# Optimization experiments

Hardware: AMD Instinct MI355X
Metric: run time of the kernel (lower is better)

The kernel has to match this reference:

```python
import jax, jax.numpy as jnp
import numpy as np

K = 16          # knn_graph k
FPS_RATIO = 0.5 # fps ratio
BN_EPS = 1e-5


def knn_idx(p, k):
    # p: [B, N, 3] -> neighbor indices [B, N, k] (loop=True: self included)
    n2 = jnp.sum(p * p, axis=-1)                                  # [B, N]
    d = n2[:, :, None] + n2[:, None, :] - 2.0 * jnp.einsum('bnc,bmc->bnm', p, p)
    _, idx = jax.lax.top_k(-d, k)                                 # smallest distances
    return idx


def gather_nbrs(x, idx):
    # x: [B, N, C], idx: [B, N, k] -> [B, N, k, C]
    return jax.vmap(lambda xb, ib: xb[ib])(x, idx)


def bn_silu(y, g, be):
    # training-mode BatchNorm over all rows (flattened) + SiLU, per PyG MLP defaults
    C = y.shape[-1]
    yf = y.reshape(-1, C)
    mu = jnp.mean(yf, axis=0)
    var = jnp.mean((yf - mu) ** 2, axis=0)
    return jax.nn.silu((y - mu) * jax.lax.rsqrt(var + BN_EPS) * g + be)


def fps_idx(p, m):
    # farthest point sampling on one cloud p: [N, 3], deterministic start at 0
    d0 = jnp.sum((p - p[0]) ** 2, axis=-1)
    def step(mind, _):
        i = jnp.argmax(mind)
        di = jnp.sum((p - p[i]) ** 2, axis=-1)
        return jnp.minimum(mind, di), i.astype(jnp.int32)
    _, idxs = jax.lax.scan(step, d0, None, length=m - 1)
    return jnp.concatenate([jnp.zeros((1,), jnp.int32), idxs])


def setup_inputs() -> dict:
    key = jax.random.key(0)
    ks = jax.random.split(key, 4)
    B, N, zdim = 16, 2048, 256
    return {
        'pos': jax.random.normal(ks[0], (B, N, 3), jnp.float32),
        'W1': jax.random.normal(ks[1], (6, 64), jnp.float32) * (1.0 / np.sqrt(6)),
        'b1': jnp.zeros((64,), jnp.float32),
        'g1': jnp.ones((64,), jnp.float32),
        'be1': jnp.zeros((64,), jnp.float32),
        'W2a': jax.random.normal(ks[2], (67, 128), jnp.float32) * (1.0 / np.sqrt(67)),
        'b2a': jnp.zeros((128,), jnp.float32),
        'g2a': jnp.ones((128,), jnp.float32),
        'be2a': jnp.zeros((128,), jnp.float32),
        'W2b': jax.random.normal(ks[3], (128, zdim), jnp.float32) * (1.0 / np.sqrt(128)),
        'b2b': jnp.zeros((zdim,), jnp.float32),
        'g2b': jnp.ones((zdim,), jnp.float32),
        'be2b': jnp.zeros((zdim,), jnp.float32),
    }


def reference(pos, W1, b1, g1, be1, W2a, b2a, g2a, be2a, W2b, b2b, g2b, be2b):
    B, N, _ = pos.shape
    M = int(N * FPS_RATIO)

    # conv1: knn graph on pos, message = MLP([x_j, pos_j - pos_i]), max-aggr
    idx1 = knn_idx(pos, K)                                  # [B, N, K]
    pos_j = gather_nbrs(pos, idx1)                          # [B, N, K, 3]
    msg = jnp.concatenate([pos_j, pos_j - pos[:, :, None, :]], axis=-1)  # [B,N,K,6]
    h = bn_silu(msg @ W1 + b1, g1, be1)                     # [B, N, K, 64]
    h = jnp.max(h, axis=2)                                  # [B, N, 64]

    # farthest point sampling, ratio 0.5
    idx_f = jax.vmap(fps_idx, in_axes=(0, None))(pos, M)    # [B, M]
    h = jax.vmap(lambda a, i: a[i])(h, idx_f)               # [B, M, 64]
    pos2 = jax.vmap(lambda a, i: a[i])(pos, idx_f)          # [B, M, 3]

    # conv2: knn on sampled points, message = MLP2([h_j, pos_j - pos_i]), max-aggr
    idx2 = knn_idx(pos2, K)                                 # [B, M, K]
    h_j = gather_nbrs(h, idx2)                              # [B, M, K, 64]
    p_j = gather_nbrs(pos2, idx2)                           # [B, M, K, 3]
    msg2 = jnp.concatenate([h_j, p_j - pos2[:, :, None, :]], axis=-1)  # [B,M,K,67]
    h2 = bn_silu(msg2 @ W2a + b2a, g2a, be2a)               # [B, M, K, 128]
    h2 = bn_silu(h2 @ W2b + b2b, g2b, be2b)                 # [B, M, K, zdim]
    h2 = jnp.max(h2, axis=2)                                # [B, M, zdim]

    # global max aggregation per cloud
    return jnp.max(h2, axis=1)                              # [B, zdim]
```

## Files before the change

kernel.cpp:

```cpp
#include <hip/hip_runtime.h>
#include <hip/hip_bf16.h>

#define NB 16
#define NN 2048
#define KNNK 16
#define MM 1024
#define RC1 (NB*NN*KNNK)
#define RC2 (NB*MM*KNNK)

typedef unsigned long long u64;
typedef __attribute__((ext_vector_type(8))) short short8;
typedef __attribute__((ext_vector_type(4))) float f32x4;

__device__ __forceinline__ float frn_mul(float a, float b){ return __fmul_rn(a,b); }
__device__ __forceinline__ float frn_add(float a, float b){ return __fadd_rn(a,b); }
__device__ __forceinline__ float frn_sub(float a, float b){ return __fsub_rn(a,b); }
__device__ __forceinline__ float silu_f(float x){ return x / (1.0f + __expf(-x)); }
__device__ __forceinline__ u64 umax64(u64 a, u64 b){ return a > b ? a : b; }

__device__ __forceinline__ unsigned f32_sortable(float f){
  unsigned u = __float_as_uint(f);
  return u ^ ((unsigned)((int)u >> 31) | 0x80000000u);
}
__device__ __forceinline__ unsigned short f2bf(float f){
  unsigned u = __float_as_uint(f);
  return (unsigned short)((u + 0x7FFFu + ((u >> 16) & 1u)) >> 16);
}
__device__ __forceinline__ float bf2f(unsigned short h){
  return __uint_as_float(((unsigned)h) << 16);
}

__device__ __forceinline__ void atomicMaxF(unsigned* addr, float v){
  if (v >= 0.f) atomicMax((int*)addr, (int)__float_as_uint(v));
  else          atomicMin(addr, __float_as_uint(v));
}
__device__ __forceinline__ void atomicMinF(unsigned* addr, float v){
  if (v >= 0.f) atomicMin((int*)addr, (int)__float_as_uint(v));
  else          atomicMax(addr, __float_as_uint(v));
}

__global__ __launch_bounds__(256) void init_kernel(float* stats1, float* stats2a, float* stats2b,
                                                   unsigned* gmax, unsigned* gmin){
  int t = blockIdx.x*256 + threadIdx.x;
  if (t < 128) stats1[t] = 0.f;
  if (t < 256) stats2a[t] = 0.f;
  if (t < 512) stats2b[t] = 0.f;
  if (t < 4096){ gmax[t] = 0xFF800000u; gmin[t] = 0x7F800000u; }
}

template<int CNT>
__device__ __forceinline__ void knn_scan(const float4* pts, int jbase,
                                         float xi, float yi, float zi, float n2i, u64* best){
#pragma unroll
  for (int p = 0; p < KNNK; ++p) best[p] = ~0ull;
  for (int jj = 0; jj < CNT; ++jj){
    float4 v = pts[jbase + jj];
    float e = frn_add(frn_add(frn_mul(xi,v.x), frn_mul(yi,v.y)), frn_mul(zi,v.z));
    float d = frn_sub(frn_add(n2i, v.w), frn_mul(2.0f, e));
    u64 key = ((u64)f32_sortable(d) << 32) | (unsigned)(jbase + jj);
    if (key < best[KNNK-1]){
      u64 cur = key;
#pragma unroll
      for (int p = 0; p < KNNK; ++p){
        u64 mn = best[p] < cur ? best[p] : cur;
        u64 mx = best[p] < cur ? cur : best[p];
        best[p] = mn; cur = mx;
      }
    }
  }
}

__global__ __launch_bounds__(256) void k0_fps_knn1(const float* __restrict__ pos,
    int* __restrict__ idxf, float* __restrict__ pos2, int* __restrict__ idx1,
    const float* __restrict__ W1, const float* __restrict__ b1, float* __restrict__ stats1){
  __shared__ __align__(16) char smem[74*1024];
  int tid = threadIdx.x;
  if (blockIdx.x < 16){
    int b = blockIdx.x;
    float4* pts4 = (float4*)smem;
    int* sel = (int*)(smem + 32*1024);
    u64* wred = (u64*)(smem + 36*1024);
    const float* pb = pos + (size_t)b*NN*3;
    float X[8], Y[8], Z[8], MD[8];
    unsigned LO[8];
#pragma unroll
    for (int q = 0; q < 8; ++q){
      int p = tid + 256*q;
      float x = pb[p*3+0], y = pb[p*3+1], z = pb[p*3+2];
      X[q] = x; Y[q] = y; Z[q] = z;
      LO[q] = ~(unsigned)p;
      pts4[p] = make_float4(x, y, z, 0.f);
    }
    float qx = pb[0], qy = pb[1], qz = pb[2];
#pragma unroll
    for (int q = 0; q < 8; ++q){
      float dx = frn_sub(X[q],qx), dy = frn_sub(Y[q],qy), dz = frn_sub(Z[q],qz);
      MD[q] = frn_add(frn_add(frn_mul(dx,dx), frn_mul(dy,dy)), frn_mul(dz,dz));
    }
    if (tid == 0) sel[0] = 0;
    int wv = tid >> 6;
    __syncthreads();
    for (int s = 1; s < MM; ++s){
      u64 t0 = umax64(((u64)__float_as_uint(MD[0])<<32)|LO[0], ((u64)__float_as_uint(MD[1])<<32)|LO[1]);
      u64 t1 = umax64(((u64)__float_as_uint(MD[2])<<32)|LO[2], ((u64)__float_as_uint(MD[3])<<32)|LO[3]);
      u64 t2 = umax64(((u64)__float_as_uint(MD[4])<<32)|LO[4], ((u64)__float_as_uint(MD[5])<<32)|LO[5]);
      u64 t3 = umax64(((u64)__float_as_uint(MD[6])<<32)|LO[6], ((u64)__float_as_uint(MD[7])<<32)|LO[7]);
      u64 kk = umax64(umax64(t0, t1), umax64(t2, t3));
#define RED_DPP(CTRL) { \
      unsigned lo_ = (unsigned)kk, hi_ = (unsigned)(kk>>32); \
      unsigned plo = (unsigned)__builtin_amdgcn_update_dpp((int)lo_,(int)lo_,CTRL,0xF,0xF,false); \
      unsigned phi = (unsigned)__builtin_amdgcn_update_dpp((int)hi_,(int)hi_,CTRL,0xF,0xF,false); \
      u64 o = ((u64)phi<<32)|plo; kk = o > kk ? o : kk; }
      RED_DPP(0xB1)
      RED_DPP(0x4E)
      RED_DPP(0x124)
      RED_DPP(0x128)
      RED_DPP(0x142)
      RED_DPP(0x143)
#undef RED_DPP
      int par = s & 1;
      if ((tid & 63) == 63) wred[par*4 + wv] = kk;
      __syncthreads();
      const u64* wr = wred + par*4;
      u64 K = umax64(umax64(wr[0], wr[1]), umax64(wr[2], wr[3]));
      unsigned wp = ~(unsigned)K;
      if (tid == 0) sel[s] = (int)wp;
      float4 wc = pts4[wp];
#pragma unroll
      for (int q = 0; q < 8; ++q){
        float dx = frn_sub(X[q],wc.x), dy = frn_sub(Y[q],wc.y), dz = frn_sub(Z[q],wc.z);
        float d = frn_add(frn_add(frn_mul(dx,dx), frn_mul(dy,dy)), frn_mul(dz,dz));
        MD[q] = fminf(MD[q], d);
      }
    }
    __syncthreads();
    for (int m = tid; m < MM; m += 256){
      int j = sel[m];
      idxf[b*MM + m] = j;
      float4 c = pts4[j];
      pos2[(size_t)(b*MM+m)*3+0] = c.x;
      pos2[(size_t)(b*MM+m)*3+1] = c.y;
      pos2[(size_t)(b*MM+m)*3+2] = c.z;
    }
  } else {
    int cid = blockIdx.x - 16;
    int b = cid >> 4;
    int rb16 = cid & 15;
    float4* pts4 = (float4*)smem;
    u64* cres = (u64*)(smem + 32*1024);
    int* idxl = (int*)(smem + 64*1024);
    float* red = (float*)(smem + 72*1024);
    const float* pb = pos + (size_t)b*NN*3;
    for (int i = tid; i < NN; i += 256){
      float x = pb[i*3+0], y = pb[i*3+1], z = pb[i*3+2];
      float n2 = frn_add(frn_add(frn_mul(x,x), frn_mul(y,y)), frn_mul(z,z));
      pts4[i] = make_float4(x, y, z, n2);
    }
    __syncthreads();
    int lrow = tid & 127;
    int ch = tid >> 7;
    int i = rb16*128 + lrow;
    float4 qv = pts4[i];
    u64 best[KNNK];
    knn_scan<1024>(pts4, ch*1024, qv.x, qv.y, qv.z, qv.w, best);
#pragma unroll
    for (int p = 0; p < KNNK; ++p) cres[tid*KNNK + p] = best[p];
    __syncthreads();
    if (tid < 128){
      const u64* A = cres + tid*KNNK;
      const u64* B = cres + (tid + 128)*KNNK;
      int ia = 0, ib = 0;
      int* op = idx1 + ((size_t)(b*NN + rb16*128 + tid))*KNNK;
#pragma unroll
      for (int p = 0; p < KNNK; ++p){
        u64 ka = A[ia], kb = B[ib];
        int v;
        if (ka < kb){ v = (int)(unsigned)ka; ++ia; }
        else        { v = (int)(unsigned)kb; ++ib; }
        op[p] = v;
        idxl[tid*KNNK + p] = v;
      }
    }
    __syncthreads();
    int lane = tid & 63, wv = tid >> 6;
    float w[6];
#pragma unroll
    for (int f = 0; f < 6; ++f) w[f] = W1[f*64 + lane];
    float bias = b1[lane];
    float ssum = 0.f, ssq = 0.f;
    for (int r = 0; r < 32; ++r){
      int lr = wv*32 + r;
      float4 pi = pts4[rb16*128 + lr];
      const int* ip = idxl + lr*KNNK;
#pragma unroll 4
      for (int k = 0; k < KNNK; ++k){
        int j = ip[k];
        float4 pj = pts4[j];
        float y = bias;
        y = fmaf(pj.x, w[0], y); y = fmaf(pj.y, w[1], y); y = fmaf(pj.z, w[2], y);
        y = fmaf(pj.x - pi.x, w[3], y); y = fmaf(pj.y - pi.y, w[4], y); y = fmaf(pj.z - pi.z, w[5], y);
        ssum += y; ssq = fmaf(y, y, ssq);
      }
    }
    red[(wv*64+lane)*2+0] = ssum; red[(wv*64+lane)*2+1] = ssq;
    __syncthreads();
    if (tid < 64){
      float s = red[(0*64+lane)*2]+red[(1*64+lane)*2]+red[(2*64+lane)*2]+red[(3*64+lane)*2];
      float q = red[(0*64+lane)*2+1]+red[(1*64+lane)*2+1]+red[(2*64+lane)*2+1]+red[(3*64+lane)*2+1];
      atomicAdd(&stats1[lane], s);
      atomicAdd(&stats1[64+lane], q);
    }
  }
}

__global__ __launch_bounds__(256) void k1_knn2_c1apply(
    const float* __restrict__ pos2, int* __restrict__ idx2,
    const float* __restrict__ pos, const int* __restrict__ idx1,
    const float* __restrict__ W1, const float* __restrict__ b1,
    const float* __restrict__ g1, const float* __restrict__ be1,
    const float* __restrict__ stats1, float* __restrict__ h){
  __shared__ __align__(16) char smem[48*1024];
  int tid = threadIdx.x;
  if (blockIdx.x < 256){
    int b = blockIdx.x >> 4;
    int rb = blockIdx.x & 15;
    float4* sm = (float4*)smem;
    u64* cres = (u64*)(smem + 16*1024);
    const float* pb = pos2 + (size_t)b*MM*3;
    for (int t = tid; t < MM; t += 256){
      float x = pb[t*3+0], y = pb[t*3+1], z = pb[t*3+2];
      float n2 = frn_add(frn_add(frn_mul(x,x), frn_mul(y,y)), frn_mul(z,z));
      sm[t] = make_float4(x, y, z, n2);
    }
    __syncthreads();
    int trow = tid & 63, ch = tid >> 6;
    int i = rb*64 + trow;
    float4 qv = sm[i];
    u64 best[KNNK];
    knn_scan<256>(sm, ch*256, qv.x, qv.y, qv.z, qv.w, best);
#pragma unroll
    for (int p = 0; p < KNNK; ++p) cres[tid*KNNK + p] = best[p];
    __syncthreads();
    if (tid < 64){
      const u64* L0 = cres + tid*KNNK;
      const u64* L1 = cres + (64 + tid)*KNNK;
      const u64* L2 = cres + (128 + tid)*KNNK;
      const u64* L3 = cres + (192 + tid)*KNNK;
      int o0=0, o1=0, o2=0, o3=0;
      int* op = idx2 + ((size_t)(b*MM + rb*64 + tid))*KNNK;
#pragma unroll
      for (int p = 0; p < KNNK; ++p){
        u64 k0 = L0[o0], k1 = L1[o1], k2 = L2[o2], k3 = L3[o3];
        u64 m01 = k0 < k1 ? k0 : k1;
        u64 m23 = k2 < k3 ? k2 : k3;
        u64 m = m01 < m23 ? m01 : m23;
        op[p] = (int)(unsigned)m;
        o0 += (m == k0); o1 += (m == k1); o2 += (m == k2); o3 += (m == k3);
      }
    }
  } else {
    int lane = tid & 63, wv = tid >> 6;
    int wave = (blockIdx.x - 256)*4 + wv;
    float w[6];
#pragma unroll
    for (int f = 0; f < 6; ++f) w[f] = W1[f*64 + lane];
    float bias = b1[lane];
    const float inv = 1.0f / (float)RC1;
    float mu = stats1[lane] * inv;
    float var = fmaxf(stats1[64+lane]*inv - mu*mu, 0.f);
    float sc = rsqrtf(var + 1e-5f) * g1[lane];
    float sh = be1[lane] - mu*sc;
    for (int r = 0; r < 8; ++r){
      int row = wave*8 + r;
      int b = row >> 11, ii = row & 2047;
      const float* pi = pos + ((size_t)(b*NN + ii))*3;
      float xi = pi[0], yi = pi[1], zi = pi[2];
      const int* ip = idx1 + (size_t)row * KNNK;
      float ymn = INFINITY, ymx = -INFINITY;
#pragma unroll 4
      for (int k = 0; k < KNNK; ++k){
        int j = ip[k];
        const float* pj = pos + ((size_t)(b*NN + j))*3;
        float xj = pj[0], yj = pj[1], zj = pj[2];
        float y = bias;
        y = fmaf(xj, w[0], y); y = fmaf(yj, w[1], y); y = fmaf(zj, w[2], y);
        y = fmaf(xj - xi, w[3], y); y = fmaf(yj - yi, w[4], y); y = fmaf(zj - zi, w[5], y);
        ymn = fminf(ymn, y); ymx = fmaxf(ymx, y);
      }
      h[((size_t)row << 6) + lane] = fmaxf(silu_f(fmaf(ymx, sc, sh)), silu_f(fmaf(ymn, sc, sh)));
    }
  }
}

__global__ __launch_bounds__(256) void conv2a_kernel(
    const float* __restrict__ h, const int* __restrict__ idxf,
    const float* __restrict__ pos2, const int* __restrict__ idx2,
    const float* __restrict__ W2a, const float* __restrict__ b2a,
    float* __restrict__ stats2a, __hip_bfloat16* __restrict__ y2a){
  __shared__ float Wl[67*128];
  __shared__ float red[4][64][4];
  for (int t = threadIdx.x; t < 67*128; t += 256) Wl[t] = W2a[t];
  __syncthreads();
  int lane = threadIdx.x & 63, wv = threadIdx.x >> 6;
  int wave = blockIdx.x*4 + wv;
  float bias0 = b2a[lane], bias1 = b2a[64+lane];
  float ssum0=0, ssq0=0, ssum1=0, ssq1=0;
  for (int r4 = 0; r4 < 16; ++r4){
    int row0 = wave*64 + r4*4;
    int b = row0 >> 14;
    int m = (row0 >> 4) & 1023;
    int j0 = idx2[row0+0], j1 = idx2[row0+1], j2 = idx2[row0+2], j3 = idx2[row0+3];
    int q0 = idxf[b*MM + j0], q1 = idxf[b*MM + j1], q2 = idxf[b*MM + j2], q3 = idxf[b*MM + j3];
    const float4* h0 = (const float4*)(h + ((size_t)(b*NN + q0) << 6));
    const float4* h1 = (const float4*)(h + ((size_t)(b*NN + q1) << 6));
    const float4* h2 = (const float4*)(h + ((size_t)(b*NN + q2) << 6));
    const float4* h3 = (const float4*)(h + ((size_t)(b*NN + q3) << 6));
    float y00=bias0, y01=bias1, y10=bias0, y11=bias1;
    float y20=bias0, y21=bias1, y30=bias0, y31=bias1;
#define C2A_STEP(e, a0v, a1v, a2v, a3v) { \
      float w0_ = Wl[(e)*128 + lane], w1_ = Wl[(e)*128 + 64 + lane]; \
      y00 = fmaf(a0v, w0_, y00); y01 = fmaf(a0v, w1_, y01); \
      y10 = fmaf(a1v, w0_, y10); y11 = fmaf(a1v, w1_, y11); \
      y20 = fmaf(a2v, w0_, y20); y21 = fmaf(a2v, w1_, y21); \
      y30 = fmaf(a3v, w0_, y30); y31 = fmaf(a3v, w1_, y31); }
#pragma unroll
    for (int f4 = 0; f4 < 16; ++f4){
      float4 v0 = h0[f4], v1 = h1[f4], v2 = h2[f4], v3 = h3[f4];
      C2A_STEP(f4*4+0, v0.x, v1.x, v2.x, v3.x)
      C2A_STEP(f4*4+1, v0.y, v1.y, v2.y, v3.y)
      C2A_STEP(f4*4+2, v0.z, v1.z, v2.z, v3.z)
      C2A_STEP(f4*4+3, v0.w, v1.w, v2.w, v3.w)
    }
    const float* pm = pos2 + ((size_t)(b*MM + m))*3;
    float pmx = pm[0], pmy = pm[1], pmz = pm[2];
    const float* pj0 = pos2 + ((size_t)(b*MM + j0))*3;
    const float* pj1 = pos2 + ((size_t)(b*MM + j1))*3;
    const float* pj2 = pos2 + ((size_t)(b*MM + j2))*3;
    const float* pj3 = pos2 + ((size_t)(b*MM + j3))*3;
    C2A_STEP(64, pj0[0]-pmx, pj1[0]-pmx, pj2[0]-pmx, pj3[0]-pmx)
    C2A_STEP(65, pj0[1]-pmy, pj1[1]-pmy, pj2[1]-pmy, pj3[1]-pmy)
    C2A_STEP(66, pj0[2]-pmz, pj1[2]-pmz, pj2[2]-pmz, pj3[2]-pmz)
#undef C2A_STEP
    ssum0 += y00+y10+y20+y30;
    ssum1 += y01+y11+y21+y31;
    ssq0 = fmaf(y00,y00,fmaf(y10,y10,fmaf(y20,y20,fmaf(y30,y30,ssq0))));
    ssq1 = fmaf(y01,y01,fmaf(y11,y11,fmaf(y21,y21,fmaf(y31,y31,ssq1))));
    y2a[(size_t)(row0+0)*128 + lane]      = __float2bfloat16(y00);
    y2a[(size_t)(row0+0)*128 + 64 + lane] = __float2bfloat16(y01);
    y2a[(size_t)(row0+1)*128 + lane]      = __float2bfloat16(y10);
    y2a[(size_t)(row0+1)*128 + 64 + lane] = __float2bfloat16(y11);
    y2a[(size_t)(row0+2)*128 + lane]      = __float2bfloat16(y20);
    y2a[(size_t)(row0+2)*128 + 64 + lane] = __float2bfloat16(y21);
    y2a[(size_t)(row0+3)*128 + lane]      = __float2bfloat16(y30);
    y2a[(size_t)(row0+3)*128 + 64 + lane] = __float2bfloat16(y31);
  }
  red[wv][lane][0]=ssum0; red[wv][lane][1]=ssq0; red[wv][lane][2]=ssum1; red[wv][lane][3]=ssq1;
  __syncthreads();
  if (threadIdx.x < 64){
    float s0=0,q0=0,s1=0,q1=0;
#pragma unroll
    for (int v2=0; v2<4; ++v2){ s0+=red[v2][lane][0]; q0+=red[v2][lane][1]; s1+=red[v2][lane][2]; q1+=red[v2][lane][3]; }
    atomicAdd(&stats2a[lane], s0);      atomicAdd(&stats2a[128+lane], q0);
    atomicAdd(&stats2a[64+lane], s1);   atomicAdd(&stats2a[192+lane], q1);
  }
}

__global__ __launch_bounds__(256) void conv2b_kernel(
    const __hip_bfloat16* __restrict__ y2a, const float* __restrict__ stats2a,
    const float* __restrict__ g2a, const float* __restrict__ be2a,
    const float* __restrict__ W2b, const float* __restrict__ b2b,
    float* __restrict__ stats2b, unsigned* __restrict__ gmax, unsigned* __restrict__ gmin){
  __shared__ __align__(16) char Albs[64*256];
  __shared__ __align__(16) char Btbs[64*256];
  __shared__ float sc2a[128], sh2a[128];
  int tid = threadIdx.x;
  int lane = tid & 63, wvi = tid >> 6;
  int ct = blockIdx.x & 3;
  int rb = blockIdx.x >> 2;
  int c0 = ct * 64;
  int batch = rb >> 5;
  if (tid < 128){
    const float inv = 1.0f / (float)RC2;
    float mu = stats2a[tid] * inv;
    float var = fmaxf(stats2a[128+tid]*inv - mu*mu, 0.f);
    float s = rsqrtf(var + 1e-5f) * g2a[tid];
    sc2a[tid] = s; sh2a[tid] = be2a[tid] - mu*s;
  }
  {
    int cc = tid & 63, u0 = tid >> 6;
#pragma unroll
    for (int i = 0; i < 4; ++i){
      int u = u0 + i*4;
      unsigned short hb[8];
#pragma unroll
      for (int e = 0; e < 8; ++e) hb[e] = f2bf(W2b[(size_t)(u*8+e)*256 + c0 + cc]);
      *(short8*)(Btbs + cc*256 + u*16) = *(short8*)hb;
    }
  }
  __syncthreads();
  short8 bfrag[4];
#pragma unroll
  for (int kb4 = 0; kb4 < 4; ++kb4){
    int col_local = wvi*16 + (lane & 15);
    bfrag[kb4] = *(short8*)(Btbs + col_local*256 + kb4*64 + (lane>>4)*16);
  }
  float bb = b2b[c0 + wvi*16 + (lane & 15)];
  float vmn = INFINITY, vmx = -INFINITY, ssum = 0.f, ssq = 0.f;
  const unsigned short* y2u = (const unsigned short*)y2a;
  int sr = tid & 63, su = tid >> 6;
  for (int tile = 0; tile < 8; ++tile){
    int row0 = rb*512 + tile*64;
    if (tile > 0) __syncthreads();
#pragma unroll
    for (int i = 0; i < 4; ++i){
      int u = su + i*4;
      short8 v = *(const short8*)(y2u + (size_t)(row0 + sr)*128 + u*8);
      unsigned short ha[8];
#pragma unroll
      for (int e = 0; e < 8; ++e){
        int k = u*8 + e;
        float f = bf2f((unsigned short)v[e]);
        ha[e] = f2bf(silu_f(fmaf(f, sc2a[k], sh2a[k])));
      }
      *(short8*)(Albs + sr*256 + ((u*16) ^ ((sr & 7) << 4))) = *(short8*)ha;
    }
    __syncthreads();
#pragma unroll
    for (int sl = 0; sl < 4; ++sl){
      f32x4 acc = {0.f, 0.f, 0.f, 0.f};
#pragma unroll
      for (int kb4 = 0; kb4 < 4; ++kb4){
        int r = sl*16 + (lane & 15);
        short8 afrag = *(short8*)(Albs + r*256 + ((kb4*64 + (lane>>4)*16) ^ ((r & 7) << 4)));
        acc = __builtin_amdgcn_mfma_f32_16x16x32_bf16(afrag, bfrag[kb4], acc, 0, 0, 0);
      }
#pragma unroll
      for (int j = 0; j < 4; ++j){
        float y = acc[j] + bb;
        vmn = fminf(vmn, y); vmx = fmaxf(vmx, y);
        ssum += y; ssq = fmaf(y, y, ssq);
      }
    }
  }
#pragma unroll
  for (int off = 16; off <= 32; off += 16){
    vmn  = fminf(vmn,  __shfl_xor(vmn,  off));
    vmx  = fmaxf(vmx,  __shfl_xor(vmx,  off));
    ssum = ssum + __shfl_xor(ssum, off);
    ssq  = ssq  + __shfl_xor(ssq,  off);
  }
  if ((lane >> 4) == 0){
    int c = c0 + wvi*16 + lane;
    atomicAdd(&stats2b[c], ssum);
    atomicAdd(&stats2b[256+c], ssq);
    atomicMaxF(&gmax[batch*256 + c], vmx);
    atomicMinF(&gmin[batch*256 + c], vmn);
  }
}

__global__ __launch_bounds__(256) void final_kernel(
    const float* __restrict__ stats2b, const unsigned* __restrict__ gmax,
    const unsigned* __restrict__ gmin, const float* __restrict__ g2b,
    const float* __restrict__ be2b, float* __restrict__ out){
  int t = blockIdx.x*256 + threadIdx.x;
  if (t >= NB*256) return;
  int c = t & 255;
  const float inv = 1.0f / (float)RC2;
  float mu = stats2b[c]*inv;
  float var = fmaxf(stats2b[256+c]*inv - mu*mu, 0.f);
  float sc = rsqrtf(var + 1e-5f)*g2b[c];
  float sh = be2b[c] - mu*sc;
  float mx = __uint_as_float(gmax[t]);
  float mn = __uint_as_float(gmin[t]);
  out[t] = fmaxf(silu_f(fmaf(mx, sc, sh)), silu_f(fmaf(mn, sc, sh)));
}

extern "C" void kernel_launch(void* const* d_in, const int* in_sizes, int n_in,
                              void* d_out, int out_size, void* d_ws, size_t ws_size,
                              hipStream_t stream){
  (void)in_sizes; (void)n_in; (void)out_size; (void)ws_size;
  const float* pos  = (const float*)d_in[0];
  const float* W1   = (const float*)d_in[1];
  const float* b1   = (const float*)d_in[2];
  const float* g1   = (const float*)d_in[3];
  const float* be1  = (const float*)d_in[4];
  const float* W2a  = (const float*)d_in[5];
  const float* b2a  = (const float*)d_in[6];
  const float* g2a  = (const float*)d_in[7];
  const float* be2a = (const float*)d_in[8];
  const float* W2b  = (const float*)d_in[9];
  const float* b2b  = (const float*)d_in[10];
  const float* g2b  = (const float*)d_in[11];
  const float* be2b = (const float*)d_in[12];

  char* w = (char*)d_ws;
  size_t off = 0;
  auto carve = [&](size_t bytes)->void*{ void* p = w + off; off += (bytes + 255) & ~(size_t)255; return p; };
  int*      idx1    = (int*)carve((size_t)NB*NN*KNNK*4);
  float*    h       = (float*)carve((size_t)NB*NN*64*4);
  int*      idxf    = (int*)carve((size_t)NB*MM*4);
  float*    pos2    = (float*)carve((size_t)NB*MM*3*4);
  int*      idx2    = (int*)carve((size_t)NB*MM*KNNK*4);
  float*    stats1  = (float*)carve(128*4);
  float*    stats2a = (float*)carve(256*4);
  float*    stats2b = (float*)carve(512*4);
  unsigned* gmax    = (unsigned*)carve(4096*4);
  unsigned* gmin    = (unsigned*)carve(4096*4);
  __hip_bfloat16* y2a = (__hip_bfloat16*)carve((size_t)RC2*128*2);

  init_kernel<<<dim3(16), dim3(256), 0, stream>>>(stats1, stats2a, stats2b, gmax, gmin);
  k0_fps_knn1<<<dim3(272), dim3(256), 0, stream>>>(pos, idxf, pos2, idx1, W1, b1, stats1);
  k1_knn2_c1apply<<<dim3(1280), dim3(256), 0, stream>>>(pos2, idx2, pos, idx1, W1, b1, g1, be1, stats1, h);
  conv2a_kernel<<<dim3(1024), dim3(256), 0, stream>>>(h, idxf, pos2, idx2, W2a, b2a, stats2a, y2a);
  conv2b_kernel<<<dim3(2048), dim3(256), 0, stream>>>(y2a, stats2a, g2a, be2a, W2b, b2b, stats2b, gmax, gmin);
  final_kernel<<<dim3(16), dim3(256), 0, stream>>>(stats2b, gmax, gmin, g2b, be2b, (float*)d_out);
}
```

Baseline: 943.3 us.

## Move conv2a to bf16 MFMA with bf16 h storage and padded LDS

Conv1 output h is now stored as bf16, and conv2a is rewritten to gather 64-row tiles of bf16 features into LDS and compute the 67x128 projection with 16x16x32 bf16 MFMA instructions instead of scalar FMAs. The weights are transposed and zero-padded to K=96 in shared memory. The BN statistics are reduced with wave shuffles. Separately, the kNN merge buffers in k0 use a stride of 17 to avoid LDS bank conflicts, which needs more shared memory. In exchange, h and the conv2a inputs lose precision.

```diff
diff --git a/kernel.cpp b/kernel.cpp
--- a/kernel.cpp
+++ b/kernel.cpp
@@ -73,7 +73,7 @@
 __global__ __launch_bounds__(256) void k0_fps_knn1(const float* __restrict__ pos,
     int* __restrict__ idxf, float* __restrict__ pos2, int* __restrict__ idx1,
     const float* __restrict__ W1, const float* __restrict__ b1, float* __restrict__ stats1){
-  __shared__ __align__(16) char smem[74*1024];
+  __shared__ __align__(16) char smem[77*1024];
   int tid = threadIdx.x;
   if (blockIdx.x < 16){
     int b = blockIdx.x;
@@ -148,8 +148,8 @@
     int rb16 = cid & 15;
     float4* pts4 = (float4*)smem;
     u64* cres = (u64*)(smem + 32*1024);
-    int* idxl = (int*)(smem + 64*1024);
-    float* red = (float*)(smem + 72*1024);
+    int* idxl = (int*)(smem + 32*1024 + 34816);
+    float* red = (float*)(smem + 32*1024 + 34816 + 8704);
     const float* pb = pos + (size_t)b*NN*3;
     for (int i = tid; i < NN; i += 256){
       float x = pb[i*3+0], y = pb[i*3+1], z = pb[i*3+2];
@@ -164,11 +164,11 @@
     u64 best[KNNK];
     knn_scan<1024>(pts4, ch*1024, qv.x, qv.y, qv.z, qv.w, best);
 #pragma unroll
-    for (int p = 0; p < KNNK; ++p) cres[tid*KNNK + p] = best[p];
+    for (int p = 0; p < KNNK; ++p) cres[tid*17 + p] = best[p];
     __syncthreads();
     if (tid < 128){
-      const u64* A = cres + tid*KNNK;
-      const u64* B = cres + (tid + 128)*KNNK;
+      const u64* A = cres + tid*17;
+      const u64* B = cres + (tid + 128)*17;
       int ia = 0, ib = 0;
       int* op = idx1 + ((size_t)(b*NN + rb16*128 + tid))*KNNK;
 #pragma unroll
@@ -178,7 +178,7 @@
         if (ka < kb){ v = (int)(unsigned)ka; ++ia; }
         else        { v = (int)(unsigned)kb; ++ib; }
         op[p] = v;
-        idxl[tid*KNNK + p] = v;
+        idxl[tid*17 + p] = v;
       }
     }
     __syncthreads();
@@ -191,7 +191,7 @@
     for (int r = 0; r < 32; ++r){
       int lr = wv*32 + r;
       float4 pi = pts4[rb16*128 + lr];
-      const int* ip = idxl + lr*KNNK;
+      const int* ip = idxl + lr*17;
 #pragma unroll 4
       for (int k = 0; k < KNNK; ++k){
         int j = ip[k];
@@ -218,7 +218,7 @@
     const float* __restrict__ pos, const int* __restrict__ idx1,
     const float* __restrict__ W1, const float* __restrict__ b1,
     const float* __restrict__ g1, const float* __restrict__ be1,
-    const float* __restrict__ stats1, float* __restrict__ h){
+    const float* __restrict__ stats1, unsigned short* __restrict__ hbf){
   __shared__ __align__(16) char smem[48*1024];
   int tid = threadIdx.x;
   if (blockIdx.x < 256){
@@ -287,81 +287,101 @@
         y = fmaf(xj - xi, w[3], y); y = fmaf(yj - yi, w[4], y); y = fmaf(zj - zi, w[5], y);
         ymn = fminf(ymn, y); ymx = fmaxf(ymx, y);
       }
-      h[((size_t)row << 6) + lane] = fmaxf(silu_f(fmaf(ymx, sc, sh)), silu_f(fmaf(ymn, sc, sh)));
+      hbf[((size_t)row << 6) + lane] = f2bf(fmaxf(silu_f(fmaf(ymx, sc, sh)), silu_f(fmaf(ymn, sc, sh))));
     }
   }
 }
 
 __global__ __launch_bounds__(256) void conv2a_kernel(
-    const float* __restrict__ h, const int* __restrict__ idxf,
+    const unsigned short* __restrict__ hbf, const int* __restrict__ idxf,
     const float* __restrict__ pos2, const int* __restrict__ idx2,
     const float* __restrict__ W2a, const float* __restrict__ b2a,
     float* __restrict__ stats2a, __hip_bfloat16* __restrict__ y2a){
-  __shared__ float Wl[67*128];
-  __shared__ float red[4][64][4];
-  for (int t = threadIdx.x; t < 67*128; t += 256) Wl[t] = W2a[t];
+  __shared__ __align__(16) unsigned short At[64*104];
+  __shared__ __align__(16) unsigned short Wt[128*104];
+  __shared__ int qs[64];
+  int tid = threadIdx.x;
+  int lane = tid & 63, wvi = tid >> 6;
+  for (int i = tid; i < 96*128; i += 256){
+    int k = i >> 7, c = i & 127;
+    Wt[c*104 + k] = (k < 67) ? f2bf(W2a[k*128 + c]) : (unsigned short)0;
+  }
+  for (int i = tid; i < 64*104/2; i += 256) ((unsigned*)At)[i] = 0u;
   __syncthreads();
-  int lane = threadIdx.x & 63, wv = threadIdx.x >> 6;
-  int wave = blockIdx.x*4 + wv;
-  float bias0 = b2a[lane], bias1 = b2a[64+lane];
-  float ssum0=0, ssq0=0, ssum1=0, ssq1=0;
-  for (int r4 = 0; r4 < 16; ++r4){
-    int row0 = wave*64 + r4*4;
-    int b = row0 >> 14;
-    int m = (row0 >> 4) & 1023;
-    int j0 = idx2[row0+0], j1 = idx2[row0+1], j2 = idx2[row0+2], j3 = idx2[row0+3];
-    int q0 = idxf[b*MM + j0], q1 = idxf[b*MM + j1], q2 = idxf[b*MM + j2], q3 = idxf[b*MM + j3];
-    const float4* h0 = (const float4*)(h + ((size_t)(b*NN + q0) << 6));
-    const float4* h1 = (const float4*)(h + ((size_t)(b*NN + q1) << 6));
-    const float4* h2 = (const float4*)(h + ((size_t)(b*NN + q2) << 6));
-    const float4* h3 = (const float4*)(h + ((size_t)(b*NN + q3) << 6));
-    float y00=bias0, y01=bias1, y10=bias0, y11=bias1;
-    float y20=bias0, y21=bias1, y30=bias0, y31=bias1;
-#define C2A_STEP(e, a0v, a1v, a2v, a3v) { \
-      float w0_ = Wl[(e)*128 + lane], w1_ = Wl[(e)*128 + 64 + lane]; \
-      y00 = fmaf(a0v, w0_, y00); y01 = fmaf(a0v, w1_, y01); \
-      y10 = fmaf(a1v, w0_, y10); y11 = fmaf(a1v, w1_, y11); \
-      y20 = fmaf(a2v, w0_, y20); y21 = fmaf(a2v, w1_, y21); \
-      y30 = fmaf(a3v, w0_, y30); y31 = fmaf(a3v, w1_, y31); }
-#pragma unroll
-    for (int f4 = 0; f4 < 16; ++f4){
-      float4 v0 = h0[f4], v1 = h1[f4], v2 = h2[f4], v3 = h3[f4];
-      C2A_STEP(f4*4+0, v0.x, v1.x, v2.x, v3.x)
-      C2A_STEP(f4*4+1, v0.y, v1.y, v2.y, v3.y)
-      C2A_STEP(f4*4+2, v0.z, v1.z, v2.z, v3.z)
-      C2A_STEP(f4*4+3, v0.w, v1.w, v2.w, v3.w)
-    }
-    const float* pm = pos2 + ((size_t)(b*MM + m))*3;
-    float pmx = pm[0], pmy = pm[1], pmz = pm[2];
-    const float* pj0 = pos2 + ((size_t)(b*MM + j0))*3;
-    const float* pj1 = pos2 + ((size_t)(b*MM + j1))*3;
-    const float* pj2 = pos2 + ((size_t)(b*MM + j2))*3;
-    const float* pj3 = pos2 + ((size_t)(b*MM + j3))*3;
-    C2A_STEP(64, pj0[0]-pmx, pj1[0]-pmx, pj2[0]-pmx, pj3[0]-pmx)
-    C2A_STEP(65, pj0[1]-pmy, pj1[1]-pmy, pj2[1]-pmy, pj3[1]-pmy)
-    C2A_STEP(66, pj0[2]-pmz, pj1[2]-pmz, pj2[2]-pmz, pj3[2]-pmz)
-#undef C2A_STEP
-    ssum0 += y00+y10+y20+y30;
-    ssum1 += y01+y11+y21+y31;
-    ssq0 = fmaf(y00,y00,fmaf(y10,y10,fmaf(y20,y20,fmaf(y30,y30,ssq0))));
-    ssq1 = fmaf(y01,y01,fmaf(y11,y11,fmaf(y21,y21,fmaf(y31,y31,ssq1))));
-    y2a[(size_t)(row0+0)*128 + lane]      = __float2bfloat16(y00);
-    y2a[(size_t)(row0+0)*128 + 64 + lane] = __float2bfloat16(y01);
-    y2a[(size_t)(row0+1)*128 + lane]      = __float2bfloat16(y10);
-    y2a[(size_t)(row0+1)*128 + 64 + lane] = __float2bfloat16(y11);
-    y2a[(size_t)(row0+2)*128 + lane]      = __float2bfloat16(y20);
-    y2a[(size_t)(row0+2)*128 + 64 + lane] = __float2bfloat16(y21);
-    y2a[(size_t)(row0+3)*128 + lane]      = __float2bfloat16(y30);
-    y2a[(size_t)(row0+3)*128 + 64 + lane] = __float2bfloat16(y31);
-  }
-  red[wv][lane][0]=ssum0; red[wv][lane][1]=ssq0; red[wv][lane][2]=ssum1; red[wv][lane][3]=ssq1;
-  __syncthreads();
-  if (threadIdx.x < 64){
-    float s0=0,q0=0,s1=0,q1=0;
-#pragma unroll
-    for (int v2=0; v2<4; ++v2){ s0+=red[v2][lane][0]; q0+=red[v2][lane][1]; s1+=red[v2][lane][2]; q1+=red[v2][lane][3]; }
-    atomicAdd(&stats2a[lane], s0);      atomicAdd(&stats2a[128+lane], q0);
-    atomicAdd(&stats2a[64+lane], s1);   atomicAdd(&stats2a[192+lane], q1);
+  int cb = wvi*32;
+  short8 bfrag[2][3];
+#pragma unroll
+  for (int cf = 0; cf < 2; ++cf)
+#pragma unroll
+    for (int kf = 0; kf < 3; ++kf){
+      int col = cb + cf*16 + (lane & 15);
+      bfrag[cf][kf] = *(short8*)(Wt + col*104 + kf*32 + (lane>>4)*8);
+    }
+  float bb[2] = { b2a[cb + (lane & 15)], b2a[cb + 16 + (lane & 15)] };
+  float ssum[2] = {0.f, 0.f}, ssq[2] = {0.f, 0.f};
+  for (int t = 0; t < 4; ++t){
+    int tbase = (blockIdx.x*4 + t)*64;
+    if (t > 0) __syncthreads();
+    if (tid < 64){
+      int grow = tbase + tid;
+      int b = grow >> 14;
+      int m = (grow >> 4) & 1023;
+      int j = idx2[grow];
+      int q = idxf[b*MM + j];
+      qs[tid] = b*NN + q;
+      const float* pm = pos2 + ((size_t)(b*MM + m))*3;
+      const float* pj = pos2 + ((size_t)(b*MM + j))*3;
+      At[tid*104 + 64] = f2bf(pj[0]-pm[0]);
+      At[tid*104 + 65] = f2bf(pj[1]-pm[1]);
+      At[tid*104 + 66] = f2bf(pj[2]-pm[2]);
+    }
+    __syncthreads();
+    {
+      int r = tid & 63, ck = tid >> 6;
+      const unsigned short* src = hbf + (size_t)qs[r]*64 + ck*16;
+      short8 v0 = *(const short8*)(src);
+      short8 v1 = *(const short8*)(src + 8);
+      *(short8*)(At + r*104 + ck*16) = v0;
+      *(short8*)(At + r*104 + ck*16 + 8) = v1;
+    }
+    __syncthreads();
+#pragma unroll
+    for (int rf = 0; rf < 4; ++rf){
+      int r = rf*16 + (lane & 15);
+      short8 af[3];
+#pragma unroll
+      for (int kf = 0; kf < 3; ++kf)
+        af[kf] = *(short8*)(At + r*104 + kf*32 + (lane>>4)*8);
+#pragma unroll
+      for (int cf = 0; cf < 2; ++cf){
+        f32x4 acc = {0.f,0.f,0.f,0.f};
+#pragma unroll
+        for (int kf = 0; kf < 3; ++kf)
+          acc = __builtin_amdgcn_mfma_f32_16x16x32_bf16(af[kf], bfrag[cf][kf], acc, 0, 0, 0);
+#pragma unroll
+        for (int jj = 0; jj < 4; ++jj){
+          int row = tbase + rf*16 + (lane>>4)*4 + jj;
+          int col = cb + cf*16 + (lane & 15);
+          float y = acc[jj] + bb[cf];
+          ssum[cf] += y; ssq[cf] = fmaf(y, y, ssq[cf]);
+          y2a[(size_t)row*128 + col] = __float2bfloat16(y);
+        }
+      }
+    }
+  }
+#pragma unroll
+  for (int cf = 0; cf < 2; ++cf){
+#pragma unroll
+    for (int off = 16; off <= 32; off += 16){
+      ssum[cf] += __shfl_xor(ssum[cf], off);
+      ssq[cf]  += __shfl_xor(ssq[cf],  off);
+    }
+  }
+  if ((lane >> 4) == 0){
+    atomicAdd(&stats2a[cb + lane], ssum[0]);
+    atomicAdd(&stats2a[128 + cb + lane], ssq[0]);
+    atomicAdd(&stats2a[cb + 16 + lane], ssum[1]);
+    atomicAdd(&stats2a[128 + cb + 16 + lane], ssq[1]);
   }
 }
 
@@ -497,7 +517,7 @@
   size_t off = 0;
   auto carve = [&](size_t bytes)->void*{ void* p = w + off; off += (bytes + 255) & ~(size_t)255; return p; };
   int*      idx1    = (int*)carve((size_t)NB*NN*KNNK*4);
-  float*    h       = (float*)carve((size_t)NB*NN*64*4);
+  unsigned short* hbf = (unsigned short*)carve((size_t)NB*NN*64*2);
   int*      idxf    = (int*)carve((size_t)NB*MM*4);
   float*    pos2    = (float*)carve((size_t)NB*MM*3*4);
   int*      idx2    = (int*)carve((size_t)NB*MM*KNNK*4);
@@ -510,8 +530,8 @@
 
   init_kernel<<<dim3(16), dim3(256), 0, stream>>>(stats1, stats2a, stats2b, gmax, gmin);
   k0_fps_knn1<<<dim3(272), dim3(256), 0, stream>>>(pos, idxf, pos2, idx1, W1, b1, stats1);
-  k1_knn2_c1apply<<<dim3(1280), dim3(256), 0, stream>>>(pos2, idx2, pos, idx1, W1, b1, g1, be1, stats1, h);
-  conv2a_kernel<<<dim3(1024), dim3(256), 0, stream>>>(h, idxf, pos2, idx2, W2a, b2a, stats2a, y2a);
+  k1_knn2_c1apply<<<dim3(1280), dim3(256), 0, stream>>>(pos2, idx2, pos, idx1, W1, b1, g1, be1, stats1, hbf);
+  conv2a_kernel<<<dim3(1024), dim3(256), 0, stream>>>(hbf, idxf, pos2, idx2, W2a, b2a, stats2a, y2a);
   conv2b_kernel<<<dim3(2048), dim3(256), 0, stream>>>(y2a, stats2a, g2a, be2a, W2b, b2b, stats2b, gmax, gmin);
   final_kernel<<<dim3(16), dim3(256), 0, stream>>>(stats2b, gmax, gmin, g2b, be2b, (float*)d_out);
 }
```

Result: faster. 825.1 us (-12.5%).
